# Kernel optimization log

Measured on AMD Instinct MI355X. Metric: run time of the kernel, lower is better.

## Reference

```python
import jax, jax.numpy as jnp
import numpy as np

DIM = 1024
HEADS = 16
HEAD_DIM = DIM // HEADS
NEG = -1e30
EPS = 1e-5


def _linear(x, w, b):
    # torch nn.Linear: y = x @ W^T + b, W: [out, in]
    return jnp.einsum('bnd,od->bno', x, w) + b


def _mha(x, ctx, wq, bq, wk, bk, wv, bv, wo, bo, mask):
    B, N, D = x.shape
    M = ctx.shape[1]
    q = _linear(x, wq, bq).reshape(B, N, HEADS, HEAD_DIM).transpose(0, 2, 1, 3)
    k = _linear(ctx, wk, bk).reshape(B, M, HEADS, HEAD_DIM).transpose(0, 2, 1, 3)
    v = _linear(ctx, wv, bv).reshape(B, M, HEADS, HEAD_DIM).transpose(0, 2, 1, 3)
    scores = jnp.einsum('bhqd,bhkd->bhqk', q, k) / np.sqrt(HEAD_DIM).astype(np.float32)
    if mask is not None:
        scores = jnp.where(mask == 0, NEG, scores)
    attn = jax.nn.softmax(scores, axis=-1)  # dropout = identity (eval mode)
    out = jnp.einsum('bhqk,bhkd->bhqd', attn, v)
    out = out.transpose(0, 2, 1, 3).reshape(B, N, D)
    return _linear(out, wo, bo)


def _ln(x, g, b):
    mu = jnp.mean(x, axis=-1, keepdims=True)
    var = jnp.mean(jnp.square(x - mu), axis=-1, keepdims=True)
    return (x - mu) * jax.lax.rsqrt(var + EPS) * g + b


def setup_inputs() -> dict:
    key = jax.random.key(0)
    ks = jax.random.split(key, 24)
    B, N, M = 2, 2048, 1024
    s = 0.02
    d = {
        'x': jax.random.normal(ks[0], (B, N, DIM), jnp.float32),
        'memory': jax.random.normal(ks[1], (B, M, DIM), jnp.float32),
        'mask': jnp.tril(jnp.ones((N, N), jnp.int32))[None, None],
    }
    i = 2
    for p in ['sa', 'ca']:
        for nm in ['q', 'k', 'v', 'o']:
            d[f'{p}_w{nm}'] = jax.random.normal(ks[i], (DIM, DIM), jnp.float32) * s; i += 1
            d[f'{p}_b{nm}'] = jnp.zeros((DIM,), jnp.float32)
    d['ff_w1'] = jax.random.normal(ks[i], (4 * DIM, DIM), jnp.float32) * s; i += 1
    d['ff_b1'] = jnp.zeros((4 * DIM,), jnp.float32)
    d['ff_w2'] = jax.random.normal(ks[i], (DIM, 4 * DIM), jnp.float32) * s; i += 1
    d['ff_b2'] = jnp.zeros((DIM,), jnp.float32)
    for j in (1, 2, 3):
        d[f'ln{j}_g'] = jnp.ones((DIM,), jnp.float32)
        d[f'ln{j}_b'] = jnp.zeros((DIM,), jnp.float32)
    return d


def reference(x, memory, mask,
              sa_wq, sa_bq, sa_wk, sa_bk, sa_wv, sa_bv, sa_wo, sa_bo,
              ca_wq, ca_bq, ca_wk, ca_bk, ca_wv, ca_bv, ca_wo, ca_bo,
              ff_w1, ff_b1, ff_w2, ff_b2,
              ln1_g, ln1_b, ln2_g, ln2_b, ln3_g, ln3_b):
    x = _ln(x + _mha(x, x, sa_wq, sa_bq, sa_wk, sa_bk, sa_wv, sa_bv, sa_wo, sa_bo, mask), ln1_g, ln1_b)
    x = _ln(x + _mha(x, memory, ca_wq, ca_bq, ca_wk, ca_bk, ca_wv, ca_bv, ca_wo, ca_bo, None), ln2_g, ln2_b)
    h = jax.nn.relu(_linear(x, ff_w1, ff_b1))  # dropout = identity (eval)
    x = _ln(x + _linear(h, ff_w2, ff_b2), ln3_g, ln3_b)
    return x
```

## Files before the change

### kernel.cpp

```cpp
#include <hip/hip_runtime.h>


typedef __attribute__((ext_vector_type(8))) short bf16x8;
typedef __attribute__((ext_vector_type(4))) float f32x4;

__device__ __forceinline__ unsigned short f2bf(float f) {
    union { float f; unsigned int u; } v; v.f = f;
    unsigned int r = v.u + 0x7fffu + ((v.u >> 16) & 1u);
    return (unsigned short)(r >> 16);
}
__device__ __forceinline__ float bf2f(unsigned short u) {
    union { unsigned int u; float f; } v; v.u = (unsigned int)u << 16;
    return v.f;
}
__device__ __forceinline__ unsigned int bftrunc(float f) {
    union { float f; unsigned int u; } v; v.f = f;
    return v.u >> 16;
}

struct ConvArgs {
    const float* src[12];
    unsigned short* dst[12];
    int blk_ofs[13];
    int n4[12];
    const float* bq; const float* bk; const float* bv;
    const float* ck; const float* cv;
    float* bqkv; float* bkvc;
};
__global__ __launch_bounds__(256) void conv_multi(ConvArgs a)
{
    int bid = blockIdx.x;
    if (bid >= a.blk_ofs[12]) {
        int i = (bid - a.blk_ofs[12]) * 256 + threadIdx.x;
        if (i < 1024)       a.bqkv[i] = a.bq[i];
        else if (i < 2048)  a.bqkv[i] = a.bk[i - 1024];
        else if (i < 3072)  a.bqkv[i] = a.bv[i - 2048];
        else if (i < 4096)  a.bkvc[i - 3072] = a.ck[i - 3072];
        else if (i < 5120)  a.bkvc[i - 3072] = a.cv[i - 4096];
        return;
    }
    int s = 0;
#pragma unroll
    for (int t = 0; t < 12; ++t) if (bid >= a.blk_ofs[t + 1]) s = t + 1;
    int i = (bid - a.blk_ofs[s]) * 256 + threadIdx.x;
    if (i >= a.n4[s]) return;
    float4 v = ((const float4*)a.src[s])[i];
    ushort4 o;
    o.x = f2bf(v.x); o.y = f2bf(v.y); o.z = f2bf(v.z); o.w = f2bf(v.w);
    ((ushort4*)a.dst[s])[i] = o;
}

template<int TM, int TN, int EPI, int SK>
__device__ __forceinline__ void gemm_body(
    unsigned short (*As)[64], unsigned short (*Bs)[64],
    const unsigned short* __restrict__ A, const unsigned short* __restrict__ W,
    const float* __restrict__ bias, unsigned short* __restrict__ out,
    int K, int Ncols, long slice_stride, int bid, int gx, int zslice)
{
    constexpr int AI = TM / 32;
    constexpr int BJ = TN / 32;

    const int tid  = threadIdx.x;
    const int lane = tid & 63;
    const int wave = tid >> 6;
    const int qd   = lane >> 4;
    const int l15  = lane & 15;
    const int wm   = (wave >> 1) * (TM / 2);
    const int wn   = (wave & 1) * (TN / 2);

    const int gpg = 8 * gx;
    const long m0 = (long)((bid / gpg) * 8 + (bid & 7)) * TM;
    const long n0 = (long)((bid % gpg) >> 3) * TN;

    f32x4 acc[AI][BJ] = {};

    const int srow = lane >> 3;
    const int scol = (((lane & 7) ^ srow)) * 8;
    const unsigned short* Ag = A + (m0 + wave * (8 * AI) + srow) * (long)K + scol;
    const unsigned short* Wg = W + (n0 + wave * (8 * BJ) + srow) * (long)K + scol;

    const int ksl   = K / SK;
    const int kbase = (SK > 1) ? zslice * ksl : 0;

    for (int k0 = kbase; k0 < kbase + ksl; k0 += 64) {
#pragma unroll
        for (int c = 0; c < AI; ++c)
            __builtin_amdgcn_global_load_lds(
                (const __attribute__((address_space(1))) unsigned int*)(Ag + (long)c * 8 * K + k0),
                (__attribute__((address_space(3))) unsigned int*)((char*)&As[0][0] + (wave * AI + c) * 1024),
                16, 0, 0);
#pragma unroll
        for (int c = 0; c < BJ; ++c)
            __builtin_amdgcn_global_load_lds(
                (const __attribute__((address_space(1))) unsigned int*)(Wg + (long)c * 8 * K + k0),
                (__attribute__((address_space(3))) unsigned int*)((char*)&Bs[0][0] + (wave * BJ + c) * 1024),
                16, 0, 0);
        __syncthreads();
#pragma unroll
        for (int kk = 0; kk < 64; kk += 32) {
            const int pg = ((((kk >> 3) + qd)) ^ (l15 & 7)) * 8;
            bf16x8 af[AI], bw[BJ];
#pragma unroll
            for (int i = 0; i < AI; ++i)
                af[i] = *(const bf16x8*)&As[wm + i * 16 + l15][pg];
#pragma unroll
            for (int j = 0; j < BJ; ++j)
                bw[j] = *(const bf16x8*)&Bs[wn + j * 16 + l15][pg];
#pragma unroll
            for (int i = 0; i < AI; ++i)
#pragma unroll
                for (int j = 0; j < BJ; ++j)
                    acc[i][j] = __builtin_amdgcn_mfma_f32_16x16x32_bf16(
                        af[i], bw[j], acc[i][j], 0, 0, 0);
        }
        __syncthreads();
    }

    unsigned short* op = out + ((SK > 1) ? (long)zslice * slice_stride : 0);
#pragma unroll
    for (int j = 0; j < BJ; ++j) {
        long col = n0 + wn + j * 16 + l15;
        float bv = (SK == 1 || zslice == 0) ? bias[col] : 0.f;
#pragma unroll
        for (int i = 0; i < AI; ++i) {
#pragma unroll
            for (int r = 0; r < 4; ++r) {
                long row = m0 + wm + i * 16 + qd * 4 + r;
                float v = acc[i][j][r] + bv;
                if (EPI == 1) v = (v > 0.f) ? v : 0.f;
                op[row * Ncols + col] = f2bf(v);
            }
        }
    }
}

template<int TM, int TN, int EPI, int SK>
__global__ __launch_bounds__(256) void gemm_bt(
    const unsigned short* __restrict__ A, const unsigned short* __restrict__ W,
    const float* __restrict__ bias, unsigned short* __restrict__ out,
    int K, int Ncols, long slice_stride)
{
    __shared__ unsigned short As[TM][64];
    __shared__ unsigned short Bs[TN][64];
    const int bid = blockIdx.y * gridDim.x + blockIdx.x;
    gemm_body<TM, TN, EPI, SK>(As, Bs, A, W, bias, out, K, Ncols, slice_stride,
                               bid, gridDim.x, (int)blockIdx.z);
}

template<int EPI, int SK>
__device__ __forceinline__ void gemm8_body(
    unsigned short* Ab, unsigned short* Bb,
    const unsigned short* __restrict__ A, const unsigned short* __restrict__ W,
    const float* __restrict__ bias, unsigned short* __restrict__ out,
    int K, int Ncols, long slice_stride, int mb, int nb, int zslice)
{
    const int tid  = threadIdx.x;
    const int lane = tid & 63;
    const int wave = tid >> 6;
    const int qd   = lane >> 4;
    const int l15  = lane & 15;
    const int wm   = (wave >> 2) * 128;
    const int wn   = (wave & 3) * 64;

    const long m0 = (long)mb * 256;
    const long n0 = (long)nb * 256;

    const int ksl   = K / SK;
    const int kbase = (SK > 1) ? zslice * ksl : 0;
    const int NG    = ksl / 64;

    f32x4 acc[8][4] = {};

    const int srow = tid >> 3;
    const int sgrp = ((tid & 7) ^ (srow & 7)) * 8;
    const unsigned short* Ag = A + (m0 + srow) * (long)K + kbase + sgrp;
    const unsigned short* Wg = W + (n0 + srow) * (long)K + kbase + sgrp;

    auto stA = [&](int db, int r0, int kt) {
        __builtin_amdgcn_global_load_lds(
            (const __attribute__((address_space(1))) unsigned int*)(Ag + (long)r0 * K + kt * 64),
            (__attribute__((address_space(3))) unsigned int*)(Ab + db * 16384 + r0 * 64 + wave * 512),
            16, 0, 0);
    };
    auto stB = [&](int db, int r0, int kt) {
        __builtin_amdgcn_global_load_lds(
            (const __attribute__((address_space(1))) unsigned int*)(Wg + (long)r0 * K + kt * 64),
            (__attribute__((address_space(3))) unsigned int*)(Bb + db * 16384 + r0 * 64 + wave * 512),
            16, 0, 0);
    };
    auto rdA = [&](int db, int row, int kk) -> bf16x8 {
        const int p = (((kk << 2) + qd) ^ (l15 & 7)) << 3;
        return *(const bf16x8*)(Ab + db * 16384 + row * 64 + p);
    };
    auto rdB = [&](int db, int row, int kk) -> bf16x8 {
        const int p = (((kk << 2) + qd) ^ (l15 & 7)) << 3;
        return *(const bf16x8*)(Bb + db * 16384 + row * 64 + p);
    };

#pragma unroll
    for (int h = 0; h < 4; ++h) stA(0, h * 64, 0);
#pragma unroll
    for (int h = 0; h < 4; ++h) stB(0, h * 64, 0);
    if (NG > 1) {
#pragma unroll
        for (int h = 0; h < 4; ++h) stA(1, h * 64, 1);
#pragma unroll
        for (int h = 0; h < 4; ++h) stB(1, h * 64, 1);
        asm volatile("s_waitcnt vmcnt(8)" ::: "memory");
    } else {
        asm volatile("s_waitcnt vmcnt(0)" ::: "memory");
    }
    __builtin_amdgcn_s_barrier();

    for (int g = 0; g < NG; ++g) {
        const int db = g & 1, nb2 = db ^ 1;
        const bool pf1 = (g >= 1) && (g + 1 < NG);
        const bool pf2 = (g + 2 < NG);
        bf16x8 af[4][2], bw[4][2];

#pragma unroll
        for (int i = 0; i < 4; ++i)
#pragma unroll
            for (int kk = 0; kk < 2; ++kk)
                af[i][kk] = rdA(db, wm + i * 16 + l15, kk);
#pragma unroll
        for (int j = 0; j < 2; ++j)
#pragma unroll
            for (int kk = 0; kk < 2; ++kk)
                bw[j][kk] = rdB(db, wn + j * 16 + l15, kk);
        if (pf1) { stA(nb2, 64, g + 1); stA(nb2, 192, g + 1); }
        __builtin_amdgcn_s_barrier();
        asm volatile("s_waitcnt lgkmcnt(0)" ::: "memory");
        __builtin_amdgcn_sched_barrier(0);
        __builtin_amdgcn_s_setprio(1);
#pragma unroll
        for (int i = 0; i < 4; ++i)
#pragma unroll
            for (int j = 0; j < 2; ++j) {
                acc[i][j] = __builtin_amdgcn_mfma_f32_16x16x32_bf16(af[i][0], bw[j][0], acc[i][j], 0, 0, 0);
                acc[i][j] = __builtin_amdgcn_mfma_f32_16x16x32_bf16(af[i][1], bw[j][1], acc[i][j], 0, 0, 0);
            }
        __builtin_amdgcn_s_setprio(0);
        __builtin_amdgcn_s_barrier();

#pragma unroll
        for (int j = 2; j < 4; ++j)
#pragma unroll
            for (int kk = 0; kk < 2; ++kk)
                bw[j][kk] = rdB(db, wn + j * 16 + l15, kk);
        if (pf1) { stB(nb2, 0, g + 1); stB(nb2, 64, g + 1); }
        __builtin_amdgcn_s_barrier();
        asm volatile("s_waitcnt lgkmcnt(0)" ::: "memory");
        __builtin_amdgcn_sched_barrier(0);
        __builtin_amdgcn_s_setprio(1);
#pragma unroll
        for (int i = 0; i < 4; ++i)
#pragma unroll
            for (int j = 2; j < 4; ++j) {
                acc[i][j] = __builtin_amdgcn_mfma_f32_16x16x32_bf16(af[i][0], bw[j][0], acc[i][j], 0, 0, 0);
                acc[i][j] = __builtin_amdgcn_mfma_f32_16x16x32_bf16(af[i][1], bw[j][1], acc[i][j], 0, 0, 0);
            }
        __builtin_amdgcn_s_setprio(0);
        __builtin_amdgcn_s_barrier();

#pragma unroll
        for (int i = 0; i < 4; ++i)
#pragma unroll
            for (int kk = 0; kk < 2; ++kk)
                af[i][kk] = rdA(db, wm + 64 + i * 16 + l15, kk);
        if (pf1) { stB(nb2, 128, g + 1); stB(nb2, 192, g + 1); }
        __builtin_amdgcn_s_barrier();
        asm volatile("s_waitcnt lgkmcnt(0)" ::: "memory");
        __builtin_amdgcn_sched_barrier(0);
        __builtin_amdgcn_s_setprio(1);
#pragma unroll
        for (int i = 0; i < 4; ++i)
#pragma unroll
            for (int j = 0; j < 2; ++j) {
                acc[4 + i][j] = __builtin_amdgcn_mfma_f32_16x16x32_bf16(af[i][0], bw[j][0], acc[4 + i][j], 0, 0, 0);
                acc[4 + i][j] = __builtin_amdgcn_mfma_f32_16x16x32_bf16(af[i][1], bw[j][1], acc[4 + i][j], 0, 0, 0);
            }
        __builtin_amdgcn_s_setprio(0);
        __builtin_amdgcn_s_barrier();

        if (pf2) { stA(db, 0, g + 2); stA(db, 128, g + 2); }
        __builtin_amdgcn_s_setprio(1);
#pragma unroll
        for (int i = 0; i < 4; ++i)
#pragma unroll
            for (int j = 2; j < 4; ++j) {
                acc[4 + i][j] = __builtin_amdgcn_mfma_f32_16x16x32_bf16(af[i][0], bw[j][0], acc[4 + i][j], 0, 0, 0);
                acc[4 + i][j] = __builtin_amdgcn_mfma_f32_16x16x32_bf16(af[i][1], bw[j][1], acc[4 + i][j], 0, 0, 0);
            }
        __builtin_amdgcn_s_setprio(0);
        if (pf2)             { asm volatile("s_waitcnt vmcnt(2)" ::: "memory"); }
        else if (g + 1 < NG) { asm volatile("s_waitcnt vmcnt(0)" ::: "memory"); }
        __builtin_amdgcn_s_barrier();
    }

    unsigned short* op = out + ((SK > 1) ? (long)zslice * slice_stride : 0);
#pragma unroll
    for (int j = 0; j < 4; ++j) {
        long col = n0 + wn + j * 16 + l15;
        float bv = (SK == 1 || zslice == 0) ? bias[col] : 0.f;
#pragma unroll
        for (int i = 0; i < 8; ++i) {
#pragma unroll
            for (int r = 0; r < 4; ++r) {
                long row = m0 + wm + (i >> 2) * 64 + (i & 3) * 16 + qd * 4 + r;
                float v = acc[i][j][r] + bv;
                if (EPI == 1) v = (v > 0.f) ? v : 0.f;
                op[row * Ncols + col] = f2bf(v);
            }
        }
    }
}

template<int EPI, int SK, int MODE>
__global__ __launch_bounds__(512) void gemm8_bt(
    const unsigned short* __restrict__ A, const unsigned short* __restrict__ W,
    const float* __restrict__ bias, unsigned short* __restrict__ out,
    int K, int Ncols, long slice_stride)
{
    extern __shared__ unsigned short smem[];
    const int bid = blockIdx.x;
    const int x = bid & 7;
    const int s = bid >> 3;
    int mb, nb, z = 0;
    if (MODE == 1) {
        mb = (x >> 1) * 4 + (s & 3);
        nb = (x & 1) * 8 + (s >> 2);
    } else {
        z  = x >> 1;
        mb = (x & 1) * 8 + (s & 7);
        nb = s >> 3;
    }
    gemm8_body<EPI, SK>(smem, smem + 32768, A, W, bias, out, K, Ncols,
                        slice_stride, mb, nb, z);
}

__global__ __launch_bounds__(512) void gemm8_dual(
    const unsigned short* A0, const unsigned short* W0, const float* b0,
    unsigned short* o0, int K0, int N0,
    const unsigned short* A1, const unsigned short* W1, const float* b1,
    unsigned short* o1, int K1, int N1)
{
    extern __shared__ unsigned short smem[];
    const int bid = blockIdx.x;
    const int x = bid & 7;
    const int s = bid >> 3;
    if (s < 24) {
        const int mb = (x >> 1) * 4 + (s & 3);
        const int nb = (x & 1) * 6 + (s >> 2);
        gemm8_body<0, 1>(smem, smem + 32768, A0, W0, b0, o0, K0, N0, 0, mb, nb, 0);
    } else {
        const int t = s - 24;
        const int mb = (x >> 1) * 2 + (t & 1);
        const int nb = (x & 1) * 4 + (t >> 1);
        gemm8_body<0, 1>(smem, smem + 32768, A1, W1, b1, o1, K1, N1, 0, mb, nb, 0);
    }
}

__global__ __launch_bounds__(256) void attn_kernel(
    const unsigned short* __restrict__ Qb, int q_stride,
    const unsigned short* __restrict__ KVb, int kv_stride, int koff, int voff,
    unsigned short* __restrict__ O,
    int Nq, int Mk, int causal)
{
    __shared__ unsigned short Ks[64][64];
    __shared__ unsigned short Vs[64][64];
    __shared__ unsigned short Ps[4][16][64];

    const int tid  = threadIdx.x;
    const int lane = tid & 63;
    const int wave = tid >> 6;
    const int qd   = lane >> 4;
    const int l15  = lane & 15;
    const int l7   = l15 & 7;
    const int h    = blockIdx.y;
    const int b    = blockIdx.z;
    int jq = blockIdx.x;
    if (causal && (b & 1)) jq = gridDim.x - 1 - jq;
    const int q0 = jq * 64;
    const int tb = q0 + wave * 16;

    bf16x8 aq0, aq1;
    {
        const unsigned short* qp =
            Qb + (long)(b * Nq + tb + l15) * q_stride + h * 64 + qd * 8;
        aq0 = *(const bf16x8*)qp;
        aq1 = *(const bf16x8*)(qp + 32);
    }

    float lpart[4] = {};
    f32x4 oacc[4] = {};

    const int krow  = tid >> 3;
    const int kcol  = (tid & 7) * 8;
    const int kcolS = (((tid & 7) ^ (krow & 7))) * 8;
    const int vj   = tid & 31;
    const int va_k = (vj & 15) + ((vj & 16) << 1);
    const int vfg  = (tid >> 5) * 8;
    const int vpc  = (va_k & 15) * 4 + (va_k >> 4);

    const unsigned short* Kg = KVb + (long)b * Mk * kv_stride + koff + h * 64;
    const unsigned short* Vg = KVb + (long)b * Mk * kv_stride + voff + h * 64;

    bf16x8 kr0, kr1, vra, vrb;
    auto prefetch = [&](int k0) {
        kr0 = *(const bf16x8*)(Kg + (long)(k0 + krow) * kv_stride + kcol);
        kr1 = *(const bf16x8*)(Kg + (long)(k0 + krow + 32) * kv_stride + kcol);
        const unsigned short* v0 = Vg + (long)(k0 + va_k) * kv_stride + vfg;
        vra = *(const bf16x8*)v0;
        vrb = *(const bf16x8*)(v0 + 16 * kv_stride);
    };

    const int nk = causal ? (q0 + 64) : Mk;
    prefetch(0);
    const float SCL = 0.125f * 1.44269504f;

    for (int k0 = 0; k0 < nk; k0 += 64) {
        __syncthreads();
        *(bf16x8*)&Ks[krow][kcolS]      = kr0;
        *(bf16x8*)&Ks[krow + 32][kcolS] = kr1;
#pragma unroll
        for (int jf = 0; jf < 8; ++jf) {
            unsigned int d = (unsigned short)vra[jf] |
                             ((unsigned int)(unsigned short)vrb[jf] << 16);
            const int row = vfg + jf;
            *(unsigned int*)&Vs[row][vpc ^ ((row & 7) << 3)] = d;
        }
        if (k0 + 64 < nk) prefetch(k0 + 64);
        __syncthreads();

        if (!causal || (k0 <= tb + 15)) {
            bf16x8 bk[4][2];
#pragma unroll
            for (int kt = 0; kt < 4; ++kt)
#pragma unroll
                for (int c = 0; c < 2; ++c)
                    bk[kt][c] = *(const bf16x8*)&Ks[kt * 16 + l15][((c * 4 + qd) ^ l7) * 8];
            f32x4 s[4];
#pragma unroll
            for (int kt = 0; kt < 4; ++kt) {
                f32x4 z = {};
                z = __builtin_amdgcn_mfma_f32_16x16x32_bf16(aq0, bk[kt][0], z, 0, 0, 0);
                z = __builtin_amdgcn_mfma_f32_16x16x32_bf16(aq1, bk[kt][1], z, 0, 0, 0);
                s[kt] = z;
            }
            const bool needmask = causal && (k0 + 63 > tb);
#pragma unroll
            for (int r = 0; r < 4; ++r) {
                const int qg = tb + qd * 4 + r;
                float e[4];
#pragma unroll
                for (int kt = 0; kt < 4; ++kt) {
                    float ev = __builtin_amdgcn_exp2f(s[kt][r] * SCL);
                    if (needmask && (k0 + kt * 16 + l15 > qg)) ev = 0.f;
                    e[kt] = ev;
                }
                lpart[r] += (e[0] + e[1]) + (e[2] + e[3]);
                unsigned int lo = bftrunc(e[0]) | (bftrunc(e[1]) << 16);
                unsigned int hi = bftrunc(e[2]) | (bftrunc(e[3]) << 16);
                uint2 pk; pk.x = lo; pk.y = hi;
                const int prow = qd * 4 + r;
                *(uint2*)&Ps[wave][prow][(l15 * 4) ^ ((prow & 7) << 3)] = pk;
            }
            bf16x8 bv[4][2];
#pragma unroll
            for (int dt = 0; dt < 4; ++dt)
#pragma unroll
                for (int c = 0; c < 2; ++c)
                    bv[dt][c] = *(const bf16x8*)&Vs[dt * 16 + l15][((c * 4 + qd) ^ l7) * 8];
            bf16x8 ap0 = *(const bf16x8*)&Ps[wave][l15][(qd ^ l7) * 8];
            bf16x8 ap1 = *(const bf16x8*)&Ps[wave][l15][((4 + qd) ^ l7) * 8];
#pragma unroll
            for (int dt = 0; dt < 4; ++dt) {
                oacc[dt] = __builtin_amdgcn_mfma_f32_16x16x32_bf16(
                    ap0, bv[dt][0], oacc[dt], 0, 0, 0);
                oacc[dt] = __builtin_amdgcn_mfma_f32_16x16x32_bf16(
                    ap1, bv[dt][1], oacc[dt], 0, 0, 0);
            }
        }
    }

#pragma unroll
    for (int r = 0; r < 4; ++r) {
        float l = lpart[r];
        l += __shfl_xor(l, 1);
        l += __shfl_xor(l, 2);
        l += __shfl_xor(l, 4);
        l += __shfl_xor(l, 8);
        float inv = 1.f / l;
        long row = (long)(b * Nq + tb + qd * 4 + r);
#pragma unroll
        for (int dt = 0; dt < 4; ++dt)
            O[row * 1024 + h * 64 + dt * 16 + l15] = f2bf(oacc[dt][r] * inv);
    }
}

template<int ND, int RESBF>
__global__ __launch_bounds__(256) void ln_res_kernel(
    const void* __restrict__ res, const unsigned short* __restrict__ delta,
    long dstride, const float* __restrict__ g, const float* __restrict__ beta,
    float* __restrict__ yout, unsigned short* __restrict__ ybf)
{
    __shared__ float red[8];
    const int row = blockIdx.x;
    const int tid = threadIdx.x;
    const long base = (long)row * 1024 + tid * 4;
    float v0, v1, v2, v3;
    if (RESBF) {
        ushort4 a = *(const ushort4*)((const unsigned short*)res + base);
        v0 = bf2f(a.x); v1 = bf2f(a.y); v2 = bf2f(a.z); v3 = bf2f(a.w);
    } else {
        float4 a = *(const float4*)((const float*)res + base);
        v0 = a.x; v1 = a.y; v2 = a.z; v3 = a.w;
    }
#pragma unroll
    for (int t = 0; t < ND; ++t) {
        ushort4 d = *(const ushort4*)(delta + t * dstride + base);
        v0 += bf2f(d.x); v1 += bf2f(d.y); v2 += bf2f(d.z); v3 += bf2f(d.w);
    }
    float s  = v0 + v1 + v2 + v3;
    float ss = v0 * v0 + v1 * v1 + v2 * v2 + v3 * v3;
#pragma unroll
    for (int off = 1; off < 64; off <<= 1) {
        s  += __shfl_xor(s, off);
        ss += __shfl_xor(ss, off);
    }
    const int wave = tid >> 6;
    if ((tid & 63) == 0) { red[wave] = s; red[4 + wave] = ss; }
    __syncthreads();
    float st  = red[0] + red[1] + red[2] + red[3];
    float sst = red[4] + red[5] + red[6] + red[7];
    float mean = st * (1.f / 1024.f);
    float var  = sst * (1.f / 1024.f) - mean * mean;
    float inv  = rsqrtf(var + 1e-5f);
    const int c = tid * 4;
    float y0 = (v0 - mean) * inv * g[c + 0] + beta[c + 0];
    float y1 = (v1 - mean) * inv * g[c + 1] + beta[c + 1];
    float y2 = (v2 - mean) * inv * g[c + 2] + beta[c + 2];
    float y3 = (v3 - mean) * inv * g[c + 3] + beta[c + 3];
    if (yout) *(float4*)(yout + base) = make_float4(y0, y1, y2, y3);
    if (ybf) {
        ushort4 o;
        o.x = f2bf(y0); o.y = f2bf(y1); o.z = f2bf(y2); o.w = f2bf(y3);
        *(ushort4*)(ybf + base) = o;
    }
}

extern "C" void kernel_launch(void* const* d_in, const int* in_sizes, int n_in,
                              void* d_out, int out_size, void* d_ws, size_t ws_size,
                              hipStream_t stream)
{
    const int B = 2, N = 2048, M = 1024, D = 1024, FF = 4096;
    const int TN = B * N;
    const int TM = B * M;
    const size_t MB = 1024 * 1024;

    const float* x     = (const float*)d_in[0];
    const float* mem   = (const float*)d_in[1];
    const float* sa_wq = (const float*)d_in[3];  const float* sa_bq = (const float*)d_in[4];
    const float* sa_wk = (const float*)d_in[5];  const float* sa_bk = (const float*)d_in[6];
    const float* sa_wv = (const float*)d_in[7];  const float* sa_bv = (const float*)d_in[8];
    const float* sa_wo = (const float*)d_in[9];  const float* sa_bo = (const float*)d_in[10];
    const float* ca_wq = (const float*)d_in[11]; const float* ca_bq = (const float*)d_in[12];
    const float* ca_wk = (const float*)d_in[13]; const float* ca_bk = (const float*)d_in[14];
    const float* ca_wv = (const float*)d_in[15]; const float* ca_bv = (const float*)d_in[16];
    const float* ca_wo = (const float*)d_in[17]; const float* ca_bo = (const float*)d_in[18];
    const float* ff_w1 = (const float*)d_in[19]; const float* ff_b1 = (const float*)d_in[20];
    const float* ff_w2 = (const float*)d_in[21]; const float* ff_b2 = (const float*)d_in[22];
    const float* ln1_g = (const float*)d_in[23]; const float* ln1_b = (const float*)d_in[24];
    const float* ln2_g = (const float*)d_in[25]; const float* ln2_b = (const float*)d_in[26];
    const float* ln3_g = (const float*)d_in[27]; const float* ln3_b = (const float*)d_in[28];

    char* w = (char*)d_ws;
    size_t off = 0;
    auto alloc = [&](size_t bytes) -> char* {
        char* p = w + off; off += (bytes + 255) & ~(size_t)255; return p;
    };

    unsigned short* xb   = (unsigned short*)alloc((size_t)TN * D * 2);
    unsigned short* memb = (unsigned short*)alloc((size_t)TM * D * 2);
    unsigned short* wqkv = (unsigned short*)alloc((size_t)3 * D * D * 2);
    unsigned short* wos  = (unsigned short*)alloc((size_t)D * D * 2);
    unsigned short* wqc  = (unsigned short*)alloc((size_t)D * D * 2);
    unsigned short* wkvc = (unsigned short*)alloc((size_t)2 * D * D * 2);
    unsigned short* woc  = (unsigned short*)alloc((size_t)D * D * 2);
    unsigned short* w1b  = (unsigned short*)alloc((size_t)FF * D * 2);
    unsigned short* w2b  = (unsigned short*)alloc((size_t)D * FF * 2);
    char* big = alloc((size_t)80 * MB);
    unsigned short* qkv   = (unsigned short*)big;
    unsigned short* ab    = (unsigned short*)(big + 24 * MB);
    unsigned short* kvb   = (unsigned short*)(big + 32 * MB);
    unsigned short* qb    = (unsigned short*)(big + 40 * MB);
    unsigned short* hb    = (unsigned short*)big;
    unsigned short* tmpbf = (unsigned short*)(big + 48 * MB);
    const long      TSL   = (long)TN * D;
    float* bqkv = (float*)alloc((size_t)3 * D * 4);
    float* bkvc = (float*)alloc((size_t)2 * D * 4);

    ConvArgs ca;
    const float* srcs[12] = {x, mem, sa_wq, sa_wk, sa_wv, sa_wo,
                             ca_wq, ca_wk, ca_wv, ca_wo, ff_w1, ff_w2};
    unsigned short* dsts[12] = {xb, memb, wqkv, wqkv + (size_t)D * D,
                                wqkv + (size_t)2 * D * D, wos, wqc, wkvc,
                                wkvc + (size_t)D * D, woc, w1b, w2b};
    long ns[12] = {(long)TN * D, (long)TM * D, (long)D * D, (long)D * D,
                   (long)D * D, (long)D * D, (long)D * D, (long)D * D,
                   (long)D * D, (long)D * D, (long)FF * D, (long)D * FF};
    int total_blk = 0;
    for (int i = 0; i < 12; ++i) {
        ca.src[i] = srcs[i]; ca.dst[i] = dsts[i];
        ca.n4[i] = (int)(ns[i] / 4);
        ca.blk_ofs[i] = total_blk;
        total_blk += (ca.n4[i] + 255) / 256;
    }
    ca.blk_ofs[12] = total_blk;
    ca.bq = sa_bq; ca.bk = sa_bk; ca.bv = sa_bv; ca.ck = ca_bk; ca.cv = ca_bv;
    ca.bqkv = bqkv; ca.bkvc = bkvc;
    conv_multi<<<dim3(total_blk + 20), dim3(256), 0, stream>>>(ca);

    dim3 blk(256);
    dim3 blk8(512);
    const unsigned int LDS8 = 131072;

    gemm8_dual<<<dim3(256), blk8, LDS8, stream>>>(
        xb,   wqkv, bqkv, qkv, D, 3 * D,
        memb, wkvc, bkvc, kvb, D, 2 * D);

    attn_kernel<<<dim3(N / 64, 16, B), blk, 0, stream>>>(
        qkv, 3 * D, qkv, 3 * D, D, 2 * D, ab, N, N, 1);
    gemm_bt<128, 64, 0, 2><<<dim3(D / 64, TN / 128, 2), blk, 0, stream>>>(
        ab, wos, sa_bo, tmpbf, D, D, TSL);
    ln_res_kernel<2, 0><<<dim3(TN), blk, 0, stream>>>(
        x, tmpbf, TSL, ln1_g, ln1_b, nullptr, xb);

    gemm_bt<128, 64, 0, 1><<<dim3(D / 64, TN / 128), blk, 0, stream>>>(
        xb, wqc, ca_bq, qb, D, D, 0);
    attn_kernel<<<dim3(N / 64, 16, B), blk, 0, stream>>>(
        qb, D, kvb, 2 * D, 0, D, ab, N, M, 0);
    gemm_bt<128, 64, 0, 2><<<dim3(D / 64, TN / 128, 2), blk, 0, stream>>>(
        ab, woc, ca_bo, tmpbf, D, D, TSL);
    ln_res_kernel<2, 1><<<dim3(TN), blk, 0, stream>>>(
        xb, tmpbf, TSL, ln2_g, ln2_b, nullptr, xb);

    gemm8_bt<1, 1, 1><<<dim3(256), blk8, LDS8, stream>>>(
        xb, w1b, ff_b1, hb, D, FF, 0);
    gemm8_bt<0, 4, 2><<<dim3(256), blk8, LDS8, stream>>>(
        hb, w2b, ff_b2, tmpbf, FF, D, TSL);
    ln_res_kernel<4, 1><<<dim3(TN), blk, 0, stream>>>(
        xb, tmpbf, TSL, ln3_g, ln3_b, (float*)d_out, nullptr);
}
```

Before: 461.2 us.

## Restructure GEMM main loop into two-phase schedule with fewer barriers

Reworks the GEMM K-loop pipeline from four quadrant phases with several barriers and lgkmcnt waits into two half-tile phases. Each phase reads all four B fragments, and the global-to-LDS prefetch of A/B halves is scheduled at new points across the double buffer. This cuts barrier and sync overhead per iteration and issues larger MFMA batches. In exchange it needs more live B fragment registers, and the correctness of the reordered buffer reuse relies on the vmcnt counts and barrier placement.

```diff
diff --git a/kernel.cpp b/kernel.cpp
--- a/kernel.cpp
+++ b/kernel.cpp
@@ -203,20 +203,19 @@
     for (int h = 0; h < 4; ++h) stB(0, h * 64, 0);
     if (NG > 1) {
 #pragma unroll
-        for (int h = 0; h < 4; ++h) stA(1, h * 64, 1);
-#pragma unroll
         for (int h = 0; h < 4; ++h) stB(1, h * 64, 1);
-        asm volatile("s_waitcnt vmcnt(8)" ::: "memory");
+        stA(1, 0, 1); stA(1, 128, 1);
+        asm volatile("s_waitcnt vmcnt(6)" ::: "memory");
     } else {
         asm volatile("s_waitcnt vmcnt(0)" ::: "memory");
     }
     __builtin_amdgcn_s_barrier();
 
     for (int g = 0; g < NG; ++g) {
-        const int db = g & 1, nb2 = db ^ 1;
-        const bool pf1 = (g >= 1) && (g + 1 < NG);
-        const bool pf2 = (g + 2 < NG);
+        const int db = g & 1, ob = db ^ 1;
         bf16x8 af[4][2], bw[4][2];
+
+        if (g + 1 < NG) { stA(ob, 64, g + 1); stA(ob, 192, g + 1); }
 
 #pragma unroll
         for (int i = 0; i < 4; ++i)
@@ -224,76 +223,43 @@
             for (int kk = 0; kk < 2; ++kk)
                 af[i][kk] = rdA(db, wm + i * 16 + l15, kk);
 #pragma unroll
-        for (int j = 0; j < 2; ++j)
+        for (int j = 0; j < 4; ++j)
 #pragma unroll
             for (int kk = 0; kk < 2; ++kk)
                 bw[j][kk] = rdB(db, wn + j * 16 + l15, kk);
-        if (pf1) { stA(nb2, 64, g + 1); stA(nb2, 192, g + 1); }
-        __builtin_amdgcn_s_barrier();
-        asm volatile("s_waitcnt lgkmcnt(0)" ::: "memory");
-        __builtin_amdgcn_sched_barrier(0);
         __builtin_amdgcn_s_setprio(1);
 #pragma unroll
         for (int i = 0; i < 4; ++i)
 #pragma unroll
-            for (int j = 0; j < 2; ++j) {
+            for (int j = 0; j < 4; ++j) {
                 acc[i][j] = __builtin_amdgcn_mfma_f32_16x16x32_bf16(af[i][0], bw[j][0], acc[i][j], 0, 0, 0);
                 acc[i][j] = __builtin_amdgcn_mfma_f32_16x16x32_bf16(af[i][1], bw[j][1], acc[i][j], 0, 0, 0);
             }
         __builtin_amdgcn_s_setprio(0);
         __builtin_amdgcn_s_barrier();
 
-#pragma unroll
-        for (int j = 2; j < 4; ++j)
-#pragma unroll
-            for (int kk = 0; kk < 2; ++kk)
-                bw[j][kk] = rdB(db, wn + j * 16 + l15, kk);
-        if (pf1) { stB(nb2, 0, g + 1); stB(nb2, 64, g + 1); }
-        __builtin_amdgcn_s_barrier();
-        asm volatile("s_waitcnt lgkmcnt(0)" ::: "memory");
-        __builtin_amdgcn_sched_barrier(0);
-        __builtin_amdgcn_s_setprio(1);
-#pragma unroll
-        for (int i = 0; i < 4; ++i)
-#pragma unroll
-            for (int j = 2; j < 4; ++j) {
-                acc[i][j] = __builtin_amdgcn_mfma_f32_16x16x32_bf16(af[i][0], bw[j][0], acc[i][j], 0, 0, 0);
-                acc[i][j] = __builtin_amdgcn_mfma_f32_16x16x32_bf16(af[i][1], bw[j][1], acc[i][j], 0, 0, 0);
-            }
-        __builtin_amdgcn_s_setprio(0);
-        __builtin_amdgcn_s_barrier();
+        if (g + 2 < NG) {
+#pragma unroll
+            for (int h = 0; h < 4; ++h) stB(db, h * 64, g + 2);
+            stA(db, 0, g + 2); stA(db, 128, g + 2);
+        }
 
 #pragma unroll
         for (int i = 0; i < 4; ++i)
 #pragma unroll
             for (int kk = 0; kk < 2; ++kk)
                 af[i][kk] = rdA(db, wm + 64 + i * 16 + l15, kk);
-        if (pf1) { stB(nb2, 128, g + 1); stB(nb2, 192, g + 1); }
-        __builtin_amdgcn_s_barrier();
-        asm volatile("s_waitcnt lgkmcnt(0)" ::: "memory");
-        __builtin_amdgcn_sched_barrier(0);
         __builtin_amdgcn_s_setprio(1);
 #pragma unroll
         for (int i = 0; i < 4; ++i)
 #pragma unroll
-            for (int j = 0; j < 2; ++j) {
+            for (int j = 0; j < 4; ++j) {
                 acc[4 + i][j] = __builtin_amdgcn_mfma_f32_16x16x32_bf16(af[i][0], bw[j][0], acc[4 + i][j], 0, 0, 0);
                 acc[4 + i][j] = __builtin_amdgcn_mfma_f32_16x16x32_bf16(af[i][1], bw[j][1], acc[4 + i][j], 0, 0, 0);
             }
         __builtin_amdgcn_s_setprio(0);
-        __builtin_amdgcn_s_barrier();
-
-        if (pf2) { stA(db, 0, g + 2); stA(db, 128, g + 2); }
-        __builtin_amdgcn_s_setprio(1);
-#pragma unroll
-        for (int i = 0; i < 4; ++i)
-#pragma unroll
-            for (int j = 2; j < 4; ++j) {
-                acc[4 + i][j] = __builtin_amdgcn_mfma_f32_16x16x32_bf16(af[i][0], bw[j][0], acc[4 + i][j], 0, 0, 0);
-                acc[4 + i][j] = __builtin_amdgcn_mfma_f32_16x16x32_bf16(af[i][1], bw[j][1], acc[4 + i][j], 0, 0, 0);
-            }
-        __builtin_amdgcn_s_setprio(0);
-        if (pf2)             { asm volatile("s_waitcnt vmcnt(2)" ::: "memory"); }
+
+        if (g + 2 < NG)      { asm volatile("s_waitcnt vmcnt(6)" ::: "memory"); }
         else if (g + 1 < NG) { asm volatile("s_waitcnt vmcnt(0)" ::: "memory"); }
         __builtin_amdgcn_s_barrier();
     }
```

Result: no change. 455.5 us (-1.2%).
